# Kernel optimization log

Hardware: AMD Instinct MI355X
Metric: run time of the kernel (lower is better)

The kernel has to match this reference:

```python
import jax, jax.numpy as jnp
import numpy as np

# Sizes (match init_kwargs / input_specs)
N, D, H, E = 4096, 512, 2048, 8   # tokens, dim, hidden_dim, num_experts
DK = 2                             # dynamic_k = top_k(3) - fixed_k(1)
NC = E - 1                         # dynamic candidate count (experts 1..7)
BETA_FIXED = 1.0 / 3.0             # fixed_k / top_k
BETA_DYN = 2.0 / 3.0               # dynamic_k / top_k


def setup_inputs() -> dict:
    key = jax.random.key(0)
    ks = jax.random.split(key, 5)
    def init(k, shape, fan_in):
        return jax.random.normal(k, shape, jnp.float32) * (1.0 / np.sqrt(fan_in))
    return {
        "x": jax.random.normal(ks[0], (N, D), jnp.float32),
        "router_W": init(ks[1], (D, NC), D),      # Linear(dim, num_non_fixed)
        "router_b": jnp.zeros((NC,), jnp.float32),
        "W1": init(ks[2], (E, D, H), D),           # per-expert first Linear
        "b1": jnp.zeros((E, H), jnp.float32),
        "W2": init(ks[3], (E, H, D), H),           # per-expert second Linear
        "b2": jnp.zeros((E, D), jnp.float32),
        "fixed_w": jnp.ones((1,), jnp.float32),    # fixed_branch_weights
    }


def reference(x, router_W, router_b, W1, b1, W2, b2, fixed_w):
    # All-expert MLP computed once (dense grouped-GEMM form of the
    # per-expert gather/MLP/scatter loop in the torch module).
    h = jax.nn.relu(jnp.einsum("nd,edh->neh", x, W1) + b1)   # [N,E,H]
    y = jnp.einsum("neh,ehd->ned", h, W2) + b2               # [N,E,D]

    # Fixed branch: expert 0 with fixed weight.
    fixed_out = fixed_w[0] * y[:, 0]                          # [N,D]

    # Dynamic branch: router over the 7 non-fixed experts.
    logits = x @ router_W + router_b                          # [N,NC]
    top_logits, top_idx = jax.lax.top_k(logits, DK)           # [N,DK]
    gates = jax.nn.softmax(top_logits, axis=-1)               # [N,DK]
    sel_expert = top_idx + 1                                  # lookup non_fixed [1..7]

    # combine weights per (token, expert): scatter gates via one-hot.
    combine = jnp.sum(jax.nn.one_hot(sel_expert, E, dtype=x.dtype)
                      * gates[..., None], axis=1)             # [N,E]
    dyn_out = jnp.einsum("ned,ne->nd", y, combine)            # [N,D]

    mixed = BETA_FIXED * fixed_out + BETA_DYN * dyn_out

    # Aux losses (same math as torch).
    importance = jax.nn.softmax(logits, axis=-1).mean(axis=0)  # [NC]
    uniform = 1.0 / NC
    load_balance_loss = jnp.mean((importance - uniform) ** 2)
    router_entropy = -jnp.sum(importance * jnp.log(jnp.clip(importance, 1e-8)))

    return mixed, load_balance_loss, router_entropy, sel_expert
```

## Files before the change

kernel.cpp:

```cpp
#include <hip/hip_runtime.h>
#include <math.h>

#define N_TOK 4096
#define DIM   512
#define HID   2048
#define NEXP  8
#define NC    7
#define OUT_MIXED (N_TOK*DIM)
#define TM    32

typedef __attribute__((ext_vector_type(8))) short bf16x8;
typedef __attribute__((ext_vector_type(4))) float f32x4;

#define XSP 520
#define HSP 264

#define OFF_TOK  4096ull
#define OFF_WT   (OFF_TOK + 131072ull)
#define OFF_XBF  (OFF_WT + 131072ull)
#define OFF_W1S  (OFF_XBF + 4194304ull)
#define OFF_W2S  (OFF_W1S + 16777216ull)
#define WS_REQ   (OFF_W2S + 16777216ull)

__device__ inline unsigned short f2bf(float f) {
  unsigned int u = __builtin_bit_cast(unsigned int, f);
  u = (u + 0x7fffu + ((u >> 16) & 1u)) >> 16;
  return (unsigned short)u;
}

__device__ void dev_convert_w(const float* __restrict__ W,
                              unsigned int* __restrict__ Ws,
                              int K, int Nm, int tiles_n, int b,
                              unsigned short (*lds)[264])
{
  const int tid = threadIdx.x;
  const int e  = b >> 7;
  const int rm = b & 127;
  const int tk = rm / tiles_n;
  const int tn = rm - tk * tiles_n;

  const float* src = W + ((size_t)e * K + tk * 32) * Nm + tn * 256;
#pragma unroll
  for (int it = 0; it < 32; ++it) {
    const int row = it, col = tid;
    lds[row][col] = f2bf(src[(size_t)row * Nm + col]);
  }
  __syncthreads();

  const int ntiles = Nm >> 4, kblks = K >> 3;
#pragma unroll
  for (int it = 0; it < 16; ++it) {
    const int uid   = it * 256 + tid;
    const int nt_l  = uid >> 8;
    const int r     = uid & 255;
    const int kb_l  = r >> 6;
    const int u     = r & 63;
    const int n_lo  = u >> 2;
    const int k_hf  = u & 3;
    const int d_l   = kb_l * 8 + k_hf * 2;
    const int h_l   = nt_l * 16 + n_lo;
    const unsigned int s0 = lds[d_l][h_l], s1 = lds[d_l + 1][h_l];
    const int nt_g = tn * 16 + nt_l;
    const int kb_g = tk * 4 + kb_l;
    const size_t frag = ((size_t)e * ntiles + nt_g) * kblks + kb_g;
    Ws[frag * 64 + n_lo * 4 + k_hf] = s0 | (s1 << 16);
  }
}

__global__ __launch_bounds__(256) void prep_kernel(
    const float* __restrict__ x, const float* __restrict__ rW,
    const float* __restrict__ rb,
    const float* __restrict__ W1, const float* __restrict__ W2,
    float* __restrict__ out,
    int* __restrict__ cpad, float* __restrict__ ipad, int* __restrict__ done,
    int* __restrict__ tok_list, float* __restrict__ wt_list,
    unsigned short* __restrict__ xbf,
    unsigned int* __restrict__ W1s, unsigned int* __restrict__ W2s)
{
  __shared__ unsigned short clds[32][264];
  __shared__ float imp_loc[8];
  __shared__ int   cnt_loc[8];
  __shared__ int   ltok[8][32];
  __shared__ float lwt[8][32];
  __shared__ int   base_s[8];

  const int tid = threadIdx.x;
  const int blk = blockIdx.x;

  if (blk >= 256) {
    const int b = blk - 256;
    if (b < 1024) {
      const int g = b * 256 + tid;
      const float* src = x + (size_t)g * 8;
      unsigned short tmp[8];
#pragma unroll
      for (int j = 0; j < 8; ++j) tmp[j] = f2bf(src[j]);
      *(uint4*)(xbf + (size_t)g * 8) = *(const uint4*)tmp;
    } else if (b < 2048) {
      dev_convert_w(W1, W1s, DIM, HID, 8, b - 1024, clds);
    } else {
      dev_convert_w(W2, W2s, HID, DIM, 2, b - 2048, clds);
    }
    return;
  }

  if (tid < 8) { imp_loc[tid] = 0.f; cnt_loc[tid] = 0; }
  __syncthreads();
  const int wave = tid >> 6, lane = tid & 63;

  for (int it = 0; it < 4; ++it) {
    const int t = blk * 16 + wave * 4 + it;
    float xv[8];
#pragma unroll
    for (int j = 0; j < 8; ++j) xv[j] = x[(size_t)t*DIM + lane + 64*j];
    float lg[NC];
#pragma unroll
    for (int e = 0; e < NC; ++e) {
      float s = 0.f;
#pragma unroll
      for (int j = 0; j < 8; ++j) s += xv[j] * rW[(lane + 64*j)*NC + e];
      lg[e] = s;
    }
#pragma unroll
    for (int e = 0; e < NC; ++e) {
      float s = lg[e];
#pragma unroll
      for (int off = 32; off > 0; off >>= 1) s += __shfl_xor(s, off, 64);
      lg[e] = s + rb[e];
    }
    int i1 = 0; float l1 = lg[0];
#pragma unroll
    for (int e = 1; e < NC; ++e) { if (lg[e] > l1) { l1 = lg[e]; i1 = e; } }
    int i2 = -1; float l2 = -3.4e38f;
#pragma unroll
    for (int e = 0; e < NC; ++e) { if (e != i1 && lg[e] > l2) { l2 = lg[e]; i2 = e; } }

    const float ed = expf(l2 - l1);
    const float g1 = 1.f/(1.f+ed), g2 = ed/(1.f+ed);

    float p[NC]; float ssum = 0.f;
#pragma unroll
    for (int e = 0; e < NC; ++e) { p[e] = expf(lg[e] - l1); ssum += p[e]; }
    const float inv = 1.f/ssum;

    if (lane == 0) {
#pragma unroll
      for (int e = 0; e < NC; ++e) atomicAdd(&imp_loc[e], p[e]*inv);
      out[OUT_MIXED + 2 + 2*t]     = (float)(i1 + 1);
      out[OUT_MIXED + 2 + 2*t + 1] = (float)(i2 + 1);
      const int e1 = i1 + 1, e2 = i2 + 1;
      int p1 = atomicAdd(&cnt_loc[e1], 1);
      ltok[e1][p1] = t;  lwt[e1][p1] = (2.f/3.f)*g1;
      int p2 = atomicAdd(&cnt_loc[e2], 1);
      ltok[e2][p2] = t;  lwt[e2][p2] = (2.f/3.f)*g2;
    }
  }
  __syncthreads();

  if (tid >= 1 && tid < 8)
    base_s[tid] = atomicAdd(&cpad[tid * 32], cnt_loc[tid]);
  if (tid < NC)
    atomicAdd(&ipad[(tid + 1) * 32], imp_loc[tid]);
  __syncthreads();

  {
    const int e = tid >> 5, i = tid & 31;
    if (e >= 1 && i < cnt_loc[e]) {
      const int dst = e * N_TOK + base_s[e] + i;
      tok_list[dst] = ltok[e][i];
      wt_list [dst] = lwt[e][i];
    }
  }

  if (tid == 0) {
    __threadfence();
    const int old = atomicAdd(done, 1);
    if (old == 255) {
      __threadfence();
      float lb = 0.f, ent = 0.f;
      for (int e = 0; e < NC; ++e) {
        float p = ipad[(e + 1) * 32] * (1.f/(float)N_TOK);
        float d = p - (1.f/(float)NC);
        lb += d*d;
        ent -= p * logf(fmaxf(p, 1e-8f));
      }
      out[OUT_MIXED]     = lb * (1.f/(float)NC);
      out[OUT_MIXED + 1] = ent;
    }
  }
}

__global__ __launch_bounds__(512) void moe_mlp_mfma(
    const unsigned short* __restrict__ xbf,
    const unsigned short* __restrict__ W1s,
    const unsigned short* __restrict__ W2s,
    const float* __restrict__ b1, const float* __restrict__ b2,
    const float* __restrict__ fixed_w,
    const int* __restrict__ cpad, const int* __restrict__ tok_list,
    const float* __restrict__ wt_list, float* __restrict__ out)
{
  const int e    = blockIdx.x >> 8;
  const int half = (blockIdx.x >> 7) & 1;
  const int tile = blockIdx.x & 127;
  const int cnt  = (e == 0) ? N_TOK : cpad[e * 32];
  const int start = tile * TM;
  if (start >= cnt) return;

  __shared__ __align__(16) unsigned short xs[32 * XSP];
  __shared__ __align__(16) unsigned short hs[32 * HSP];
  __shared__ int   tok_s[TM];
  __shared__ float wt_s[TM];

  const int tid = threadIdx.x;
  if (tid < TM) {
    int idx = start + tid; int t = 0; float w = 0.f;
    if (idx < cnt) {
      if (e == 0) { t = idx; w = (1.f/3.f) * fixed_w[0]; }
      else        { t = tok_list[e*N_TOK + idx]; w = wt_list[e*N_TOK + idx]; }
    }
    tok_s[tid] = t; wt_s[tid] = w;
  }
  __syncthreads();

  for (int i = tid; i < 32 * 64; i += 512) {
    const int m = i >> 6, cb = i & 63;
    *(uint4*)(xs + m * XSP + cb * 8) =
        *(const uint4*)(xbf + (size_t)tok_s[m] * DIM + cb * 8);
  }

  const int lane = tid & 63;
  const int w    = tid >> 6;
  const int l15  = lane & 15;
  const int q    = lane >> 4;

  const unsigned short* W1e = W1s + (size_t)e * 128 * 64 * 128;
  const unsigned short* W2e = W2s + (size_t)e * 32 * 256 * 128;

  f32x4 yacc[2][4];
#pragma unroll
  for (int mi = 0; mi < 2; ++mi)
#pragma unroll
    for (int t = 0; t < 4; ++t) yacc[mi][t] = (f32x4){0.f, 0.f, 0.f, 0.f};

  __syncthreads();

  for (int c = half * 4; c < half * 4 + 4; ++c) {
    f32x4 hacc[2][2];
#pragma unroll
    for (int mi = 0; mi < 2; ++mi)
#pragma unroll
      for (int t = 0; t < 2; ++t) hacc[mi][t] = (f32x4){0.f, 0.f, 0.f, 0.f};
    const int nt_base = c * 16 + w * 2;
#pragma unroll 4
    for (int s = 0; s < 16; ++s) {
      const bf16x8 a0 = *(const bf16x8*)(xs + l15 * XSP + s * 32 + q * 8);
      const bf16x8 a1 = *(const bf16x8*)(xs + (16 + l15) * XSP + s * 32 + q * 8);
#pragma unroll
      for (int t = 0; t < 2; ++t) {
        const bf16x8 b = *(const bf16x8*)(
            W1e + (((size_t)(nt_base + t) * 64) + s * 4 + q) * 128 + l15 * 8);
        hacc[0][t] = __builtin_amdgcn_mfma_f32_16x16x32_bf16(a0, b, hacc[0][t], 0, 0, 0);
        hacc[1][t] = __builtin_amdgcn_mfma_f32_16x16x32_bf16(a1, b, hacc[1][t], 0, 0, 0);
      }
    }
#pragma unroll
    for (int t = 0; t < 2; ++t) {
      const float bv = b1[e * HID + (nt_base + t) * 16 + l15];
      const int col = w * 32 + t * 16 + l15;
#pragma unroll
      for (int reg = 0; reg < 4; ++reg) {
        hs[(q * 4 + reg) * HSP + col]      = f2bf(fmaxf(hacc[0][t][reg] + bv, 0.f));
        hs[(16 + q * 4 + reg) * HSP + col] = f2bf(fmaxf(hacc[1][t][reg] + bv, 0.f));
      }
    }
    __syncthreads();

#pragma unroll 2
    for (int s = 0; s < 8; ++s) {
      const bf16x8 a0 = *(const bf16x8*)(hs + l15 * HSP + s * 32 + q * 8);
      const bf16x8 a1 = *(const bf16x8*)(hs + (16 + l15) * HSP + s * 32 + q * 8);
      const int kblk = c * 32 + s * 4 + q;
#pragma unroll
      for (int t = 0; t < 4; ++t) {
        const bf16x8 b = *(const bf16x8*)(
            W2e + (((size_t)(w * 4 + t) * 256) + kblk) * 128 + l15 * 8);
        yacc[0][t] = __builtin_amdgcn_mfma_f32_16x16x32_bf16(a0, b, yacc[0][t], 0, 0, 0);
        yacc[1][t] = __builtin_amdgcn_mfma_f32_16x16x32_bf16(a1, b, yacc[1][t], 0, 0, 0);
      }
    }
    __syncthreads();
  }

#pragma unroll
  for (int t = 0; t < 4; ++t) {
    const int d = (w * 4 + t) * 16 + l15;
    const float b2v = half ? 0.f : b2[e * DIM + d];
#pragma unroll
    for (int reg = 0; reg < 4; ++reg) {
      const int m0 = q * 4 + reg, m1 = 16 + q * 4 + reg;
      atomicAdd(&out[(size_t)tok_s[m0] * DIM + d], wt_s[m0] * (yacc[0][t][reg] + b2v));
      atomicAdd(&out[(size_t)tok_s[m1] * DIM + d], wt_s[m1] * (yacc[1][t][reg] + b2v));
    }
  }
}

__global__ __launch_bounds__(256) void router_only(
    const float* __restrict__ x, const float* __restrict__ rW,
    const float* __restrict__ rb, float* __restrict__ out,
    int* __restrict__ cpad, float* __restrict__ ipad, int* __restrict__ done,
    int* __restrict__ tok_list, float* __restrict__ wt_list)
{
  __shared__ float imp_loc[8];
  __shared__ int   cnt_loc[8];
  __shared__ int   ltok[8][32];
  __shared__ float lwt[8][32];
  __shared__ int   base_s[8];

  const int tid = threadIdx.x;
  if (tid < 8) { imp_loc[tid] = 0.f; cnt_loc[tid] = 0; }
  __syncthreads();
  const int wave = tid >> 6, lane = tid & 63;

  for (int it = 0; it < 4; ++it) {
    const int t = blockIdx.x * 16 + wave * 4 + it;
    float xv[8];
#pragma unroll
    for (int j = 0; j < 8; ++j) xv[j] = x[(size_t)t*DIM + lane + 64*j];
    float lg[NC];
#pragma unroll
    for (int e = 0; e < NC; ++e) {
      float s = 0.f;
#pragma unroll
      for (int j = 0; j < 8; ++j) s += xv[j] * rW[(lane + 64*j)*NC + e];
      lg[e] = s;
    }
#pragma unroll
    for (int e = 0; e < NC; ++e) {
      float s = lg[e];
#pragma unroll
      for (int off = 32; off > 0; off >>= 1) s += __shfl_xor(s, off, 64);
      lg[e] = s + rb[e];
    }
    int i1 = 0; float l1 = lg[0];
#pragma unroll
    for (int e = 1; e < NC; ++e) { if (lg[e] > l1) { l1 = lg[e]; i1 = e; } }
    int i2 = -1; float l2 = -3.4e38f;
#pragma unroll
    for (int e = 0; e < NC; ++e) { if (e != i1 && lg[e] > l2) { l2 = lg[e]; i2 = e; } }
    const float ed = expf(l2 - l1);
    const float g1 = 1.f/(1.f+ed), g2 = ed/(1.f+ed);
    float p[NC]; float ssum = 0.f;
#pragma unroll
    for (int e = 0; e < NC; ++e) { p[e] = expf(lg[e] - l1); ssum += p[e]; }
    const float inv = 1.f/ssum;
    if (lane == 0) {
#pragma unroll
      for (int e = 0; e < NC; ++e) atomicAdd(&imp_loc[e], p[e]*inv);
      out[OUT_MIXED + 2 + 2*t]     = (float)(i1 + 1);
      out[OUT_MIXED + 2 + 2*t + 1] = (float)(i2 + 1);
      const int e1 = i1 + 1, e2 = i2 + 1;
      int p1 = atomicAdd(&cnt_loc[e1], 1);
      ltok[e1][p1] = t;  lwt[e1][p1] = (2.f/3.f)*g1;
      int p2 = atomicAdd(&cnt_loc[e2], 1);
      ltok[e2][p2] = t;  lwt[e2][p2] = (2.f/3.f)*g2;
    }
  }
  __syncthreads();
  if (tid >= 1 && tid < 8)
    base_s[tid] = atomicAdd(&cpad[tid * 32], cnt_loc[tid]);
  if (tid < NC)
    atomicAdd(&ipad[(tid + 1) * 32], imp_loc[tid]);
  __syncthreads();
  {
    const int e = tid >> 5, i = tid & 31;
    if (e >= 1 && i < cnt_loc[e]) {
      const int dst = e * N_TOK + base_s[e] + i;
      tok_list[dst] = ltok[e][i];
      wt_list [dst] = lwt[e][i];
    }
  }
  if (tid == 0) {
    __threadfence();
    const int old = atomicAdd(done, 1);
    if (old == 255) {
      __threadfence();
      float lb = 0.f, ent = 0.f;
      for (int e = 0; e < NC; ++e) {
        float p = ipad[(e + 1) * 32] * (1.f/(float)N_TOK);
        float d = p - (1.f/(float)NC);
        lb += d*d;
        ent -= p * logf(fmaxf(p, 1e-8f));
      }
      out[OUT_MIXED]     = lb * (1.f/(float)NC);
      out[OUT_MIXED + 1] = ent;
    }
  }
}

__global__ __launch_bounds__(256) void moe_mlp_kernel(
    const float* __restrict__ x,
    const float* __restrict__ W1, const float* __restrict__ b1,
    const float* __restrict__ W2, const float* __restrict__ b2,
    const float* __restrict__ fixed_w,
    const int* __restrict__ cpad, const int* __restrict__ tok_list,
    const float* __restrict__ wt_list, float* __restrict__ out)
{
  const int e    = blockIdx.x >> 8;
  const int tile = blockIdx.x & 255;
  const int cnt  = (e == 0) ? N_TOK : cpad[e * 32];
  const int start = tile * 16;
  if (start >= cnt) return;

  __shared__ float xs[DIM][17];
  __shared__ float hs2[256][17];
  __shared__ int   tok_s[16];
  __shared__ float wt_s[16];

  const int tid = threadIdx.x;
  if (tid < 16) {
    int idx = start + tid; int t = 0; float w = 0.f;
    if (idx < cnt) {
      if (e == 0) { t = idx; w = (1.f/3.f) * fixed_w[0]; }
      else        { t = tok_list[e*N_TOK + idx]; w = wt_list[e*N_TOK + idx]; }
    }
    tok_s[tid] = t; wt_s[tid] = w;
  }
  __syncthreads();

  for (int i = tid; i < 16*DIM; i += 256) {
    const int m = i >> 9, d = i & (DIM-1);
    xs[d][m] = x[(size_t)tok_s[m]*DIM + d];
  }

  const int r  = tid & 63;
  const int m0 = (tid >> 6) * 4;
  const float* W1e = W1 + (size_t)e * DIM * HID;
  const float* W2e = W2 + (size_t)e * HID * DIM;
  const float* b1e = b1 + e * HID;

  float yacc[4][8];
#pragma unroll
  for (int j = 0; j < 4; ++j)
#pragma unroll
    for (int i = 0; i < 8; ++i) yacc[j][i] = 0.f;

  __syncthreads();

  for (int c = 0; c < 8; ++c) {
    const int k0 = c * 256;
    float bv[4];
#pragma unroll
    for (int i = 0; i < 4; ++i) bv[i] = b1e[k0 + r + 64*i];
    float hacc[4][4];
#pragma unroll
    for (int j = 0; j < 4; ++j)
#pragma unroll
      for (int i = 0; i < 4; ++i) hacc[j][i] = bv[i];
#pragma unroll 2
    for (int d = 0; d < DIM; ++d) {
      float wv[4];
#pragma unroll
      for (int i = 0; i < 4; ++i) wv[i] = W1e[(size_t)d*HID + k0 + r + 64*i];
      float xv[4];
#pragma unroll
      for (int j = 0; j < 4; ++j) xv[j] = xs[d][m0+j];
#pragma unroll
      for (int j = 0; j < 4; ++j)
#pragma unroll
        for (int i = 0; i < 4; ++i) hacc[j][i] += xv[j]*wv[i];
    }
#pragma unroll
    for (int i = 0; i < 4; ++i)
#pragma unroll
      for (int j = 0; j < 4; ++j) hs2[r + 64*i][m0+j] = fmaxf(hacc[j][i], 0.f);
    __syncthreads();

#pragma unroll 2
    for (int k = 0; k < 256; ++k) {
      float wv2[8];
#pragma unroll
      for (int i = 0; i < 8; ++i) wv2[i] = W2e[(size_t)(k0+k)*DIM + r + 64*i];
      float hv[4];
#pragma unroll
      for (int j = 0; j < 4; ++j) hv[j] = hs2[k][m0+j];
#pragma unroll
      for (int j = 0; j < 4; ++j)
#pragma unroll
        for (int i = 0; i < 8; ++i) yacc[j][i] += hv[j]*wv2[i];
    }
    __syncthreads();
  }

#pragma unroll
  for (int i = 0; i < 8; ++i) {
    const int d = r + 64*i;
    const float b2v = b2[e*DIM + d];
#pragma unroll
    for (int j = 0; j < 4; ++j) {
      const int m = m0 + j;
      atomicAdd(&out[(size_t)tok_s[m]*DIM + d], wt_s[m]*(yacc[j][i] + b2v));
    }
  }
}

extern "C" void kernel_launch(void* const* d_in, const int* in_sizes, int n_in,
                              void* d_out, int out_size, void* d_ws, size_t ws_size,
                              hipStream_t stream)
{
  const float* x  = (const float*)d_in[0];
  const float* rW = (const float*)d_in[1];
  const float* rb = (const float*)d_in[2];
  const float* W1 = (const float*)d_in[3];
  const float* b1 = (const float*)d_in[4];
  const float* W2 = (const float*)d_in[5];
  const float* b2 = (const float*)d_in[6];
  const float* fw = (const float*)d_in[7];
  float* out = (float*)d_out;

  int*   cpad     = (int*)d_ws;
  float* ipad     = (float*)((char*)d_ws + 1024);
  int*   done     = (int*)((char*)d_ws + 2048);
  int*   tok_list = (int*)((char*)d_ws + OFF_TOK);
  float* wt_list  = (float*)((char*)d_ws + OFF_WT);

  hipMemsetAsync(d_ws, 0, 4096, stream);
  hipMemsetAsync(d_out, 0, (size_t)OUT_MIXED*4, stream);

  if (ws_size >= WS_REQ) {
    unsigned short* xbf = (unsigned short*)((char*)d_ws + OFF_XBF);
    unsigned int*   W1s = (unsigned int*)((char*)d_ws + OFF_W1S);
    unsigned int*   W2s = (unsigned int*)((char*)d_ws + OFF_W2S);
    prep_kernel<<<3328, 256, 0, stream>>>(x, rW, rb, W1, W2, out,
                                          cpad, ipad, done, tok_list, wt_list,
                                          xbf, W1s, W2s);
    moe_mlp_mfma<<<NEXP*2*128, 512, 0, stream>>>(xbf, (const unsigned short*)W1s,
                                                 (const unsigned short*)W2s, b1, b2, fw,
                                                 cpad, tok_list, wt_list, out);
  } else {
    router_only<<<256, 256, 0, stream>>>(x, rW, rb, out, cpad, ipad, done,
                                         tok_list, wt_list);
    moe_mlp_kernel<<<NEXP*256, 256, 0, stream>>>(x, W1, b1, W2, b2, fw,
                                                 cpad, tok_list, wt_list, out);
  }
}
```

Before: 288.2 us.

## Enlarge MFMA token tile to 48, fuse x bf16 conversion into MLP kernel

Raises the per-block token tile from 32 to 48 rows (three 16-row MFMA fragments), so each weight fragment loaded from global memory feeds more MFMAs. The separate x-to-bf16 prep pass is removed; the MLP kernel now gathers fp32 token rows and converts them in LDS, in two K-halves to fit the smaller LDS buffer. Weight conversion now uses float4 loads, and the block grid is re-indexed with interleaved halves. This costs more registers and repeats the x conversion in every hidden chunk and in both halves.

```diff
diff --git a/kernel.cpp b/kernel.cpp
--- a/kernel.cpp
+++ b/kernel.cpp
@@ -7,12 +7,13 @@
 #define NEXP  8
 #define NC    7
 #define OUT_MIXED (N_TOK*DIM)
-#define TM    32
+#define TM    48
+#define TPE   86
 
 typedef __attribute__((ext_vector_type(8))) short bf16x8;
 typedef __attribute__((ext_vector_type(4))) float f32x4;
 
-#define XSP 520
+#define XSP 264
 #define HSP 264
 
 #define OFF_TOK  4096ull
@@ -41,9 +42,13 @@
 
   const float* src = W + ((size_t)e * K + tk * 32) * Nm + tn * 256;
 #pragma unroll
-  for (int it = 0; it < 32; ++it) {
-    const int row = it, col = tid;
-    lds[row][col] = f2bf(src[(size_t)row * Nm + col]);
+  for (int it = 0; it < 8; ++it) {
+    const int g   = it * 256 + tid;
+    const int row = g >> 6, c4 = g & 63;
+    const float4 v = *(const float4*)(src + (size_t)row * Nm + c4 * 4);
+    ushort4 o;
+    o.x = f2bf(v.x); o.y = f2bf(v.y); o.z = f2bf(v.z); o.w = f2bf(v.w);
+    *(ushort4*)(&lds[row][c4 * 4]) = o;
   }
   __syncthreads();
 
@@ -74,7 +79,6 @@
     float* __restrict__ out,
     int* __restrict__ cpad, float* __restrict__ ipad, int* __restrict__ done,
     int* __restrict__ tok_list, float* __restrict__ wt_list,
-    unsigned short* __restrict__ xbf,
     unsigned int* __restrict__ W1s, unsigned int* __restrict__ W2s)
 {
   __shared__ unsigned short clds[32][264];
@@ -89,18 +93,8 @@
 
   if (blk >= 256) {
     const int b = blk - 256;
-    if (b < 1024) {
-      const int g = b * 256 + tid;
-      const float* src = x + (size_t)g * 8;
-      unsigned short tmp[8];
-#pragma unroll
-      for (int j = 0; j < 8; ++j) tmp[j] = f2bf(src[j]);
-      *(uint4*)(xbf + (size_t)g * 8) = *(const uint4*)tmp;
-    } else if (b < 2048) {
-      dev_convert_w(W1, W1s, DIM, HID, 8, b - 1024, clds);
-    } else {
-      dev_convert_w(W2, W2s, HID, DIM, 2, b - 2048, clds);
-    }
+    if (b < 1024) dev_convert_w(W1, W1s, DIM, HID, 8, b, clds);
+    else          dev_convert_w(W2, W2s, HID, DIM, 2, b - 1024, clds);
     return;
   }
 
@@ -191,7 +185,7 @@
 }
 
 __global__ __launch_bounds__(512) void moe_mlp_mfma(
-    const unsigned short* __restrict__ xbf,
+    const float* __restrict__ x,
     const unsigned short* __restrict__ W1s,
     const unsigned short* __restrict__ W2s,
     const float* __restrict__ b1, const float* __restrict__ b2,
@@ -199,15 +193,16 @@
     const int* __restrict__ cpad, const int* __restrict__ tok_list,
     const float* __restrict__ wt_list, float* __restrict__ out)
 {
-  const int e    = blockIdx.x >> 8;
-  const int half = (blockIdx.x >> 7) & 1;
-  const int tile = blockIdx.x & 127;
+  const int e    = blockIdx.x / (TPE * 2);
+  const int r    = blockIdx.x % (TPE * 2);
+  const int tile = r >> 1;
+  const int half = r & 1;
   const int cnt  = (e == 0) ? N_TOK : cpad[e * 32];
   const int start = tile * TM;
   if (start >= cnt) return;
 
-  __shared__ __align__(16) unsigned short xs[32 * XSP];
-  __shared__ __align__(16) unsigned short hs[32 * HSP];
+  __shared__ __align__(16) unsigned short xs[TM * XSP];
+  __shared__ __align__(16) unsigned short hs[TM * HSP];
   __shared__ int   tok_s[TM];
   __shared__ float wt_s[TM];
 
@@ -222,12 +217,6 @@
   }
   __syncthreads();
 
-  for (int i = tid; i < 32 * 64; i += 512) {
-    const int m = i >> 6, cb = i & 63;
-    *(uint4*)(xs + m * XSP + cb * 8) =
-        *(const uint4*)(xbf + (size_t)tok_s[m] * DIM + cb * 8);
-  }
-
   const int lane = tid & 63;
   const int w    = tid >> 6;
   const int l15  = lane & 15;
@@ -236,42 +225,63 @@
   const unsigned short* W1e = W1s + (size_t)e * 128 * 64 * 128;
   const unsigned short* W2e = W2s + (size_t)e * 32 * 256 * 128;
 
-  f32x4 yacc[2][4];
-#pragma unroll
-  for (int mi = 0; mi < 2; ++mi)
+  f32x4 yacc[3][4];
+#pragma unroll
+  for (int mi = 0; mi < 3; ++mi)
 #pragma unroll
     for (int t = 0; t < 4; ++t) yacc[mi][t] = (f32x4){0.f, 0.f, 0.f, 0.f};
 
-  __syncthreads();
-
   for (int c = half * 4; c < half * 4 + 4; ++c) {
-    f32x4 hacc[2][2];
-#pragma unroll
-    for (int mi = 0; mi < 2; ++mi)
+    const int nt_base = c * 16 + w * 2;
+    f32x4 hacc[3][2];
+#pragma unroll
+    for (int mi = 0; mi < 3; ++mi)
 #pragma unroll
       for (int t = 0; t < 2; ++t) hacc[mi][t] = (f32x4){0.f, 0.f, 0.f, 0.f};
-    const int nt_base = c * 16 + w * 2;
+
+#pragma unroll
+    for (int kh = 0; kh < 2; ++kh) {
+      for (int i = tid; i < TM * 32; i += 512) {
+        const int m = i >> 5, cb = i & 31;
+        const float* src = x + (size_t)tok_s[m] * DIM + kh * 256 + cb * 8;
+        const float4 v0 = *(const float4*)(src);
+        const float4 v1 = *(const float4*)(src + 4);
+        ushort4 o0, o1;
+        o0.x=f2bf(v0.x); o0.y=f2bf(v0.y); o0.z=f2bf(v0.z); o0.w=f2bf(v0.w);
+        o1.x=f2bf(v1.x); o1.y=f2bf(v1.y); o1.z=f2bf(v1.z); o1.w=f2bf(v1.w);
+        *(ushort4*)(xs + m * XSP + cb * 8)     = o0;
+        *(ushort4*)(xs + m * XSP + cb * 8 + 4) = o1;
+      }
+      __syncthreads();
+
 #pragma unroll 4
-    for (int s = 0; s < 16; ++s) {
-      const bf16x8 a0 = *(const bf16x8*)(xs + l15 * XSP + s * 32 + q * 8);
-      const bf16x8 a1 = *(const bf16x8*)(xs + (16 + l15) * XSP + s * 32 + q * 8);
-#pragma unroll
-      for (int t = 0; t < 2; ++t) {
-        const bf16x8 b = *(const bf16x8*)(
-            W1e + (((size_t)(nt_base + t) * 64) + s * 4 + q) * 128 + l15 * 8);
-        hacc[0][t] = __builtin_amdgcn_mfma_f32_16x16x32_bf16(a0, b, hacc[0][t], 0, 0, 0);
-        hacc[1][t] = __builtin_amdgcn_mfma_f32_16x16x32_bf16(a1, b, hacc[1][t], 0, 0, 0);
+      for (int s = 0; s < 8; ++s) {
+        const bf16x8 a0 = *(const bf16x8*)(xs + l15 * XSP + s * 32 + q * 8);
+        const bf16x8 a1 = *(const bf16x8*)(xs + (16 + l15) * XSP + s * 32 + q * 8);
+        const bf16x8 a2 = *(const bf16x8*)(xs + (32 + l15) * XSP + s * 32 + q * 8);
+        const int kblk = (kh * 8 + s) * 4 + q;
+#pragma unroll
+        for (int t = 0; t < 2; ++t) {
+          const bf16x8 b = *(const bf16x8*)(
+              W1e + (((size_t)(nt_base + t) * 64) + kblk) * 128 + l15 * 8);
+          hacc[0][t] = __builtin_amdgcn_mfma_f32_16x16x32_bf16(a0, b, hacc[0][t], 0, 0, 0);
+          hacc[1][t] = __builtin_amdgcn_mfma_f32_16x16x32_bf16(a1, b, hacc[1][t], 0, 0, 0);
+          hacc[2][t] = __builtin_amdgcn_mfma_f32_16x16x32_bf16(a2, b, hacc[2][t], 0, 0, 0);
+        }
       }
-    }
+      if (kh == 0) __syncthreads();
+    }
+
 #pragma unroll
     for (int t = 0; t < 2; ++t) {
       const float bv = b1[e * HID + (nt_base + t) * 16 + l15];
       const int col = w * 32 + t * 16 + l15;
 #pragma unroll
-      for (int reg = 0; reg < 4; ++reg) {
-        hs[(q * 4 + reg) * HSP + col]      = f2bf(fmaxf(hacc[0][t][reg] + bv, 0.f));
-        hs[(16 + q * 4 + reg) * HSP + col] = f2bf(fmaxf(hacc[1][t][reg] + bv, 0.f));
-      }
+      for (int mi = 0; mi < 3; ++mi)
+#pragma unroll
+        for (int reg = 0; reg < 4; ++reg)
+          hs[(mi * 16 + q * 4 + reg) * HSP + col] =
+              f2bf(fmaxf(hacc[mi][t][reg] + bv, 0.f));
     }
     __syncthreads();
 
@@ -279,6 +289,7 @@
     for (int s = 0; s < 8; ++s) {
       const bf16x8 a0 = *(const bf16x8*)(hs + l15 * HSP + s * 32 + q * 8);
       const bf16x8 a1 = *(const bf16x8*)(hs + (16 + l15) * HSP + s * 32 + q * 8);
+      const bf16x8 a2 = *(const bf16x8*)(hs + (32 + l15) * HSP + s * 32 + q * 8);
       const int kblk = c * 32 + s * 4 + q;
 #pragma unroll
       for (int t = 0; t < 4; ++t) {
@@ -286,6 +297,7 @@
             W2e + (((size_t)(w * 4 + t) * 256) + kblk) * 128 + l15 * 8);
         yacc[0][t] = __builtin_amdgcn_mfma_f32_16x16x32_bf16(a0, b, yacc[0][t], 0, 0, 0);
         yacc[1][t] = __builtin_amdgcn_mfma_f32_16x16x32_bf16(a1, b, yacc[1][t], 0, 0, 0);
+        yacc[2][t] = __builtin_amdgcn_mfma_f32_16x16x32_bf16(a2, b, yacc[2][t], 0, 0, 0);
       }
     }
     __syncthreads();
@@ -296,11 +308,12 @@
     const int d = (w * 4 + t) * 16 + l15;
     const float b2v = half ? 0.f : b2[e * DIM + d];
 #pragma unroll
-    for (int reg = 0; reg < 4; ++reg) {
-      const int m0 = q * 4 + reg, m1 = 16 + q * 4 + reg;
-      atomicAdd(&out[(size_t)tok_s[m0] * DIM + d], wt_s[m0] * (yacc[0][t][reg] + b2v));
-      atomicAdd(&out[(size_t)tok_s[m1] * DIM + d], wt_s[m1] * (yacc[1][t][reg] + b2v));
-    }
+    for (int mi = 0; mi < 3; ++mi)
+#pragma unroll
+      for (int reg = 0; reg < 4; ++reg) {
+        const int m = mi * 16 + q * 4 + reg;
+        atomicAdd(&out[(size_t)tok_s[m] * DIM + d], wt_s[m] * (yacc[mi][t][reg] + b2v));
+      }
   }
 }
 
@@ -527,13 +540,12 @@
   hipMemsetAsync(d_out, 0, (size_t)OUT_MIXED*4, stream);
 
   if (ws_size >= WS_REQ) {
-    unsigned short* xbf = (unsigned short*)((char*)d_ws + OFF_XBF);
-    unsigned int*   W1s = (unsigned int*)((char*)d_ws + OFF_W1S);
-    unsigned int*   W2s = (unsigned int*)((char*)d_ws + OFF_W2S);
-    prep_kernel<<<3328, 256, 0, stream>>>(x, rW, rb, W1, W2, out,
+    unsigned int* W1s = (unsigned int*)((char*)d_ws + OFF_W1S);
+    unsigned int* W2s = (unsigned int*)((char*)d_ws + OFF_W2S);
+    prep_kernel<<<2304, 256, 0, stream>>>(x, rW, rb, W1, W2, out,
                                           cpad, ipad, done, tok_list, wt_list,
-                                          xbf, W1s, W2s);
-    moe_mlp_mfma<<<NEXP*2*128, 512, 0, stream>>>(xbf, (const unsigned short*)W1s,
+                                          W1s, W2s);
+    moe_mlp_mfma<<<NEXP*TPE*2, 512, 0, stream>>>(x, (const unsigned short*)W1s,
                                                  (const unsigned short*)W2s, b1, b2, fw,
                                                  cpad, tok_list, wt_list, out);
   } else {
```

Result: slower. 388.1 us (+34.7%).
